# Kernel tuning notes

Hardware: AMD Instinct MI355X
Metric: run time of the kernel (lower is better)

## Reference

```python
import jax, jax.numpy as jnp
import numpy as np

B, LQ, LK = 8, 512, 512
DQ = DK = DV = 512
H = 128


def setup_inputs() -> dict:
    key = jax.random.key(0)
    kq, kk, kv, k1, k2, k3 = jax.random.split(key, 6)
    query = jax.random.normal(kq, (B, LQ, DQ), dtype=jnp.float32)
    key_t = jax.random.normal(kk, (B, LK, DK), dtype=jnp.float32)
    value = jax.random.normal(kv, (B, LK, DV), dtype=jnp.float32)
    # Linear weights stored torch-style as (out_features, in_features)
    w1 = jax.random.normal(k1, (H, DQ), dtype=jnp.float32) / np.sqrt(DQ)
    w2 = jax.random.normal(k2, (H, DK), dtype=jnp.float32) / np.sqrt(DK)
    v = jax.random.normal(k3, (1, H), dtype=jnp.float32) / np.sqrt(H)
    return {"query": query, "key": key_t, "value": value, "w1": w1, "w2": w2, "v": v}


def reference(query, key, value, w1, w2, v):
    # Linear projections first (mathematically identical to projecting the
    # broadcast tensors, since Linear is linear): (B,Lq,H), (B,Lk,H)
    q_proj = jnp.einsum("bqd,hd->bqh", query, w1)
    k_proj = jnp.einsum("bkd,hd->bkh", key, w2)
    # Broadcast add -> tanh -> project to scalar: (B,Lq,Lk,H) intermediate
    feat = jnp.tanh(q_proj[:, :, None, :] + k_proj[:, None, :, :])
    score = jnp.einsum("bqkh,h->bqk", feat, v[0])
    attention_weights = jax.nn.softmax(score, axis=-1)
    context_vector = jnp.einsum("bqk,bkv->bqv", attention_weights, value)
    return (attention_weights, context_vector)
```

## Files before the change

kernel.cpp:

```cpp
#include <hip/hip_runtime.h>

#define TWO_LOG2E 2.8853900817779268f

__device__ __forceinline__ float frcp(float x) {
#if __has_builtin(__builtin_amdgcn_rcpf)
  return __builtin_amdgcn_rcpf(x);
#else
  return 1.0f / x;
#endif
}
__device__ __forceinline__ float fexp2(float x) {
#if __has_builtin(__builtin_amdgcn_exp2f)
  return __builtin_amdgcn_exp2f(x);
#else
  return exp2f(x);
#endif
}
__device__ __forceinline__ unsigned short f2bf(float f) {
  unsigned int u = __float_as_uint(f);
  u += 0x7fffu + ((u >> 16) & 1u);
  return (unsigned short)(u >> 16);
}
__device__ __forceinline__ unsigned int pack2bf(float lo, float hi) {
  return (unsigned int)f2bf(lo) | ((unsigned int)f2bf(hi) << 16);
}

using short8 = __attribute__((ext_vector_type(8))) short;
using f32x4v = __attribute__((ext_vector_type(4))) float;
using f32x8s = __attribute__((ext_vector_type(8))) float;
using f32x2 = __attribute__((ext_vector_type(2))) float;

__device__ __forceinline__ f32x2 pkfma(f32x2 a, f32x2 b, f32x2 c) {
  return __builtin_elementwise_fma(a, b, c);
}
__device__ __forceinline__ f32x2 splat2(float x) {
  f32x2 r;
  r.x = x;
  r.y = x;
  return r;
}
__device__ __forceinline__ f32x2 unpack_bf2(unsigned u) {
  f32x2 r;
  r.x = __uint_as_float(u << 16);
  r.y = __uint_as_float(u & 0xffff0000u);
  return r;
}
__device__ __forceinline__ void cell4k(float a0, float a1, float a2, float a3,
                                       f32x2 b0, f32x2 b1, f32x2 b2, f32x2 b3,
                                       float v0, float v1, float v2, float v3,
                                       f32x2& s) {
  const f32x2 one = {1.f, 1.f};
  f32x2 x0 = pkfma(splat2(a0), b0, one);
  f32x2 x1 = pkfma(splat2(a1), b1, one);
  f32x2 x2 = pkfma(splat2(a2), b2, one);
  f32x2 x3 = pkfma(splat2(a3), b3, one);
  f32x2 p01 = x0 * x1, p23 = x2 * x3;
  f32x2 n01 = pkfma(splat2(v0), x1, splat2(v1) * x0);
  f32x2 n23 = pkfma(splat2(v2), x3, splat2(v3) * x2);
  f32x2 num = pkfma(n01, p23, n23 * p01);
  f32x2 den = p01 * p23;
  f32x2 r;
  r.x = frcp(den.x);
  r.y = frcp(den.y);
  s = pkfma(num, r, s);
}

__global__ __launch_bounds__(256) void k_pre(
    const float* __restrict__ query, const float* __restrict__ key,
    const float* __restrict__ w1, const float* __restrict__ w2,
    const float* __restrict__ value,
    float* __restrict__ Aout, unsigned short* __restrict__ BoutT,
    unsigned short* __restrict__ valT) {
  __shared__ __align__(16) char Abuf[16 * 128];
  __shared__ __align__(16) char Bbuf[128 * 128];
  __shared__ unsigned short ts[64][66];

  const int t = threadIdx.x;

  if (blockIdx.y == 0) {
    const int px = blockIdx.x;
    const bool isB = px >= 256;
    const float* in = isB ? key : query;
    const float* wm = isB ? w2 : w1;
    const int m0g = (px & 255) * 16;
    const int w = t >> 6, l = t & 63;

    f32x4v acc[2];
    acc[0] = 0;
    acc[1] = 0;

    float4 aS;
    float4 wS[4][2];

#define P_LOAD(k0_)                                                        \
  {                                                                        \
    aS = *(const float4*)&in[(m0g + (t >> 4)) * 512 + (k0_) + (t & 15) * 4]; \
    _Pragma("unroll") for (int i = 0; i < 4; ++i) {                        \
      int tt = t + i * 256;                                                \
      int row = tt >> 3, g = tt & 7;                                       \
      const float* src = &wm[row * 512 + (k0_) + g * 8];                   \
      wS[i][0] = *(const float4*)src;                                      \
      wS[i][1] = *(const float4*)(src + 4);                                \
    }                                                                      \
  }
#define P_WRITE()                                                          \
  {                                                                        \
    int arow = t >> 4, q4 = t & 15;                                        \
    *(uint2*)(Abuf + arow * 128 + (((q4 >> 1) ^ (arow & 7)) << 4) +        \
              ((q4 & 1) << 3)) =                                           \
        make_uint2(pack2bf(aS.x, aS.y), pack2bf(aS.z, aS.w));              \
    _Pragma("unroll") for (int i = 0; i < 4; ++i) {                        \
      int tt = t + i * 256;                                                \
      int row = tt >> 3, g = tt & 7;                                       \
      uint4 p = make_uint4(                                                \
          pack2bf(wS[i][0].x, wS[i][0].y), pack2bf(wS[i][0].z, wS[i][0].w),\
          pack2bf(wS[i][1].x, wS[i][1].y), pack2bf(wS[i][1].z, wS[i][1].w));\
      *(uint4*)(Bbuf + row * 128 + ((g ^ (row & 7)) << 4)) = p;            \
    }                                                                      \
  }

    P_LOAD(0);
#pragma unroll
    for (int ks8 = 0; ks8 < 8; ++ks8) {
      if (ks8) __syncthreads();
      P_WRITE();
      if (ks8 < 7) P_LOAD(ks8 * 64 + 64);
      __syncthreads();
#pragma unroll
      for (int ks = 0; ks < 2; ++ks) {
        const int gb = ks * 4 + (l >> 4);
        const int ra = l & 15;
        short8 af = *(const short8*)(Abuf + ra * 128 + ((gb ^ (ra & 7)) << 4));
#pragma unroll
        for (int ni = 0; ni < 2; ++ni) {
          const int rb = w * 32 + ni * 16 + (l & 15);
          short8 bf_ = *(const short8*)(Bbuf + rb * 128 + ((gb ^ (rb & 7)) << 4));
          if (isB)
            acc[ni] = __builtin_amdgcn_mfma_f32_16x16x32_bf16(bf_, af, acc[ni], 0, 0, 0);
          else
            acc[ni] = __builtin_amdgcn_mfma_f32_16x16x32_bf16(af, bf_, acc[ni], 0, 0, 0);
        }
      }
    }
#undef P_LOAD
#undef P_WRITE
    if (!isB) {
#pragma unroll
      for (int ni = 0; ni < 2; ++ni) {
        int col = w * 32 + ni * 16 + (l & 15);
#pragma unroll
        for (int j = 0; j < 4; ++j) {
          int row = m0g + (l >> 4) * 4 + j;
          Aout[row * 128 + col] = fexp2(acc[ni][j] * TWO_LOG2E);
        }
      }
    } else {
      int m = m0g + (l & 15);
#pragma unroll
      for (int ni = 0; ni < 2; ++ni)
#pragma unroll
        for (int j = 0; j < 4; ++j) {
          int h = w * 32 + ni * 16 + (l >> 4) * 4 + j;
          BoutT[h * 4096 + m] = f2bf(fexp2(acc[ni][j] * TWO_LOG2E));
        }
    }
  } else {
    const int x = blockIdx.x;
    const int b = x >> 6, k0 = ((x >> 3) & 7) * 64, n0 = (x & 7) * 64;
    {
      int kr = t >> 4, n4 = (t & 15) * 4;
#pragma unroll
      for (int i = 0; i < 4; ++i) {
        float4 f =
            *(const float4*)&value[((b * 512) + k0 + kr + 16 * i) * 512 + n0 + n4];
        *(ushort4*)&ts[kr + 16 * i][n4] =
            make_ushort4(f2bf(f.x), f2bf(f.y), f2bf(f.z), f2bf(f.w));
      }
    }
    __syncthreads();
    {
      int nw = t >> 4, k4 = (t & 15) * 4;
#pragma unroll
      for (int i = 0; i < 4; ++i) {
        int n = nw + 16 * i;
        ushort4 o = make_ushort4(ts[k4 + 0][n], ts[k4 + 1][n], ts[k4 + 2][n],
                                 ts[k4 + 3][n]);
        *(ushort4*)&valT[((b * 512) + n0 + n) * 512 + k0 + k4] = o;
      }
    }
  }
}

__global__ __launch_bounds__(512, 8) void k_score_softmax(
    const float* __restrict__ Aexp, const unsigned short* __restrict__ BexpT,
    const float* __restrict__ vw, float* __restrict__ attn,
    unsigned short* __restrict__ attnBf) {
  __shared__ __align__(16) f32x2 part[512][4];
  __shared__ float red[8][4];

  const int tid = threadIdx.x;
  const int b = blockIdx.y;
  const int qbase = blockIdx.x * 4;
  const int wav = tid >> 6;
  const int hgrp = wav >> 2;
  const int kq = wav & 3;
  const int lane = tid & 63;

  const unsigned* const bbase32 = (const unsigned*)(BexpT + b * 512);
  const int kidx = kq * 64 + lane;

  const float* const pa0 =
      Aexp + __builtin_amdgcn_readfirstlane((b * 512 + qbase) * 128);
  const float* const pa1 = pa0 + 128;
  const float* const pa2 = pa0 + 256;
  const float* const pa3 = pa0 + 384;
  const float* const pv = vw;
  const unsigned hoff = (unsigned)__builtin_amdgcn_readfirstlane(hgrp * 256);

  f32x2 acc0 = {0.f, 0.f}, acc1 = {0.f, 0.f};
  f32x2 acc2 = {0.f, 0.f}, acc3 = {0.f, 0.f};

#pragma unroll
  for (int ch = 0; ch < 8; ++ch) {
    f32x8s sa0, sa1, sa2, sa3, sv;
    unsigned soff = hoff + (unsigned)(ch * 32);
    asm volatile(
        "s_load_dwordx8 %0, %5, %10\n\t"
        "s_load_dwordx8 %1, %6, %10\n\t"
        "s_load_dwordx8 %2, %7, %10\n\t"
        "s_load_dwordx8 %3, %8, %10\n\t"
        "s_load_dwordx8 %4, %9, %10"
        : "=&s"(sa0), "=&s"(sa1), "=&s"(sa2), "=&s"(sa3), "=&s"(sv)
        : "s"(pa0), "s"(pa1), "s"(pa2), "s"(pa3), "s"(pv), "s"(soff));

    unsigned u[8];
#pragma unroll
    for (int j = 0; j < 8; ++j)
      u[j] = bbase32[hgrp * 131072 + ch * 16384 + j * 2048 + kidx];

    asm volatile("s_waitcnt lgkmcnt(0)"
                 : "+s"(sa0), "+s"(sa1), "+s"(sa2), "+s"(sa3), "+s"(sv));

#pragma unroll
    for (int g = 0; g < 2; ++g) {
      f32x2 b0 = unpack_bf2(u[g * 4 + 0]);
      f32x2 b1 = unpack_bf2(u[g * 4 + 1]);
      f32x2 b2 = unpack_bf2(u[g * 4 + 2]);
      f32x2 b3 = unpack_bf2(u[g * 4 + 3]);
      const int h = g * 4;
      cell4k(sa0[h], sa0[h + 1], sa0[h + 2], sa0[h + 3], b0, b1, b2, b3,
             sv[h], sv[h + 1], sv[h + 2], sv[h + 3], acc0);
      cell4k(sa1[h], sa1[h + 1], sa1[h + 2], sa1[h + 3], b0, b1, b2, b3,
             sv[h], sv[h + 1], sv[h + 2], sv[h + 3], acc1);
      cell4k(sa2[h], sa2[h + 1], sa2[h + 2], sa2[h + 3], b0, b1, b2, b3,
             sv[h], sv[h + 1], sv[h + 2], sv[h + 3], acc2);
      cell4k(sa3[h], sa3[h + 1], sa3[h + 2], sa3[h + 3], b0, b1, b2, b3,
             sv[h], sv[h + 1], sv[h + 2], sv[h + 3], acc3);
    }
  }

  part[tid][0] = acc0;
  part[tid][1] = acc1;
  part[tid][2] = acc2;
  part[tid][3] = acc3;
  __syncthreads();
  {
    const f32x2* pp = part[tid ^ 256];
    acc0 += pp[0];
    acc1 += pp[1];
    acc2 += pp[2];
    acc3 += pp[3];
  }

  float P0e = fexp2(acc0.x * -TWO_LOG2E);
  float P0o = fexp2(acc0.y * -TWO_LOG2E);
  float P1e = fexp2(acc1.x * -TWO_LOG2E);
  float P1o = fexp2(acc1.y * -TWO_LOG2E);
  float P2e = fexp2(acc2.x * -TWO_LOG2E);
  float P2o = fexp2(acc2.y * -TWO_LOG2E);
  float P3e = fexp2(acc3.x * -TWO_LOG2E);
  float P3o = fexp2(acc3.y * -TWO_LOG2E);
  float s0 = P0e + P0o, s1 = P1e + P1o, s2 = P2e + P2o, s3 = P3e + P3o;
#pragma unroll
  for (int off = 32; off > 0; off >>= 1) {
    s0 += __shfl_xor(s0, off);
    s1 += __shfl_xor(s1, off);
    s2 += __shfl_xor(s2, off);
    s3 += __shfl_xor(s3, off);
  }
  if (lane == 0) {
    red[wav][0] = s0; red[wav][1] = s1; red[wav][2] = s2; red[wav][3] = s3;
  }
  __syncthreads();
  const int rb = hgrp * 4;
  float r0 = frcp(red[rb][0] + red[rb + 1][0] + red[rb + 2][0] + red[rb + 3][0]);
  float r1 = frcp(red[rb][1] + red[rb + 1][1] + red[rb + 2][1] + red[rb + 3][1]);
  float r2 = frcp(red[rb][2] + red[rb + 1][2] + red[rb + 2][2] + red[rb + 3][2]);
  float r3 = frcp(red[rb][3] + red[rb + 1][3] + red[rb + 2][3] + red[rb + 3][3]);

  const int row0 = (b * 512 + qbase) * 512;
  const int k0 = kidx * 2;
  if (hgrp == 0) {
    float a0e = P0e * r0, a0o = P0o * r0, a1e = P1e * r1, a1o = P1o * r1;
    *(float2*)&attn[row0 + k0] = make_float2(a0e, a0o);
    *(float2*)&attn[row0 + 512 + k0] = make_float2(a1e, a1o);
    *(unsigned*)&attnBf[row0 + k0] = pack2bf(a0e, a0o);
    *(unsigned*)&attnBf[row0 + 512 + k0] = pack2bf(a1e, a1o);
  } else {
    float a2e = P2e * r2, a2o = P2o * r2, a3e = P3e * r3, a3o = P3o * r3;
    *(float2*)&attn[row0 + 1024 + k0] = make_float2(a2e, a2o);
    *(float2*)&attn[row0 + 1536 + k0] = make_float2(a3e, a3o);
    *(unsigned*)&attnBf[row0 + 1024 + k0] = pack2bf(a2e, a2o);
    *(unsigned*)&attnBf[row0 + 1536 + k0] = pack2bf(a3e, a3o);
  }
}

__global__ __launch_bounds__(256) void k_context_mfma(
    const unsigned short* __restrict__ attnBf,
    const unsigned short* __restrict__ valT, float* __restrict__ ctx) {
  __shared__ __align__(16) char At[64 * 128];
  __shared__ __align__(16) char Bt[32 * 128];

  const int t = threadIdx.x;
  const int b = blockIdx.z;
  const int m0 = blockIdx.y * 64, n0 = blockIdx.x * 32;
  const int w = t >> 6, l = t & 63;
  const int wr = w >> 1, wc = w & 1;

  f32x4v acc[2];
  acc[0] = 0;
  acc[1] = 0;

  const int sr = t >> 2;
  const int sg = (t & 3);
  const int sswz = sr & 7;
  const int rbs = t >> 3;
  const int gbs = t & 7;

  for (int k0 = 0; k0 < 512; k0 += 64) {
    if (k0) __syncthreads();
    {
      const unsigned short* srca = &attnBf[(b * 512 + m0 + sr) * 512 + k0];
      char* dst = At + sr * 128;
#pragma unroll
      for (int h = 0; h < 2; ++h) {
        int g = sg * 2 + h;
        uint4 va = *(const uint4*)(srca + g * 8);
        *(uint4*)(dst + ((g ^ sswz) << 4)) = va;
      }
      uint4 vb = *(const uint4*)&valT[(b * 512 + n0 + rbs) * 512 + k0 + gbs * 8];
      *(uint4*)(Bt + rbs * 128 + ((gbs ^ (rbs & 7)) << 4)) = vb;
    }
    __syncthreads();
#pragma unroll
    for (int ks = 0; ks < 2; ++ks) {
      const int gb = ks * 4 + (l >> 4);
      const int rb = wc * 16 + (l & 15);
      short8 bf_ = *(const short8*)(Bt + rb * 128 + ((gb ^ (rb & 7)) << 4));
#pragma unroll
      for (int mi = 0; mi < 2; ++mi) {
        int ra = wr * 32 + mi * 16 + (l & 15);
        short8 af = *(const short8*)(At + ra * 128 + ((gb ^ (ra & 7)) << 4));
        acc[mi] = __builtin_amdgcn_mfma_f32_16x16x32_bf16(af, bf_, acc[mi], 0, 0, 0);
      }
    }
  }
  __syncthreads();
#pragma unroll
  for (int mi = 0; mi < 2; ++mi) {
    int col = n0 + wc * 16 + (l & 15);
#pragma unroll
    for (int j = 0; j < 4; ++j) {
      int row = m0 + wr * 32 + mi * 16 + (l >> 4) * 4 + j;
      ctx[(b * 512 + row) * 512 + col] = acc[mi][j];
    }
  }
}

extern "C" void kernel_launch(void* const* d_in, const int* in_sizes, int n_in,
                              void* d_out, int out_size, void* d_ws, size_t ws_size,
                              hipStream_t stream) {
  const float* query = (const float*)d_in[0];
  const float* key   = (const float*)d_in[1];
  const float* value = (const float*)d_in[2];
  const float* w1    = (const float*)d_in[3];
  const float* w2    = (const float*)d_in[4];
  const float* v     = (const float*)d_in[5];

  float* attn = (float*)d_out;
  float* ctx  = attn + 8 * 512 * 512;

  float* Aexp = (float*)d_ws;
  unsigned short* BexpT = (unsigned short*)(Aexp + 4096 * 128);
  unsigned short* valT = BexpT + 128 * 4096;
  unsigned short* attnBf = valT + 8 * 512 * 512;

  k_pre<<<dim3(512, 2), 256, 0, stream>>>(query, key, w1, w2, value,
                                          Aexp, BexpT, valT);
  k_score_softmax<<<dim3(128, 8), 512, 0, stream>>>(Aexp, BexpT, v, attn, attnBf);
  k_context_mfma<<<dim3(16, 8, 8), 256, 0, stream>>>(attnBf, valT, ctx);
}
```

Before: 52.21 us.

## Process eight query rows per block in score-softmax kernel to reuse key loads

The score/softmax kernel now computes eight query rows per block instead of four. Each block loads the bf16 key-projection data once and reuses it across twice as many rows, which halves that traffic per row. The scalar loads use immediate offsets from a per-head-group base pointer. The grid is halved and launch bounds are lowered to 4 blocks per SIMD/CU. More accumulators and SGPRs are live per thread, so occupancy and latency hiding may drop.

```diff
diff --git a/kernel.cpp b/kernel.cpp
--- a/kernel.cpp
+++ b/kernel.cpp
@@ -191,16 +191,16 @@
   }
 }
 
-__global__ __launch_bounds__(512, 8) void k_score_softmax(
+__global__ __launch_bounds__(512, 4) void k_score_softmax(
     const float* __restrict__ Aexp, const unsigned short* __restrict__ BexpT,
     const float* __restrict__ vw, float* __restrict__ attn,
     unsigned short* __restrict__ attnBf) {
-  __shared__ __align__(16) f32x2 part[512][4];
-  __shared__ float red[8][4];
+  __shared__ __align__(16) f32x2 part[512][8];
+  __shared__ float red[8][8];
 
   const int tid = threadIdx.x;
   const int b = blockIdx.y;
-  const int qbase = blockIdx.x * 4;
+  const int qbase = blockIdx.x * 8;
   const int wav = tid >> 6;
   const int hgrp = wav >> 2;
   const int kq = wav & 3;
@@ -208,110 +208,143 @@
 
   const unsigned* const bbase32 = (const unsigned*)(BexpT + b * 512);
   const int kidx = kq * 64 + lane;
-
-  const float* const pa0 =
-      Aexp + __builtin_amdgcn_readfirstlane((b * 512 + qbase) * 128);
-  const float* const pa1 = pa0 + 128;
-  const float* const pa2 = pa0 + 256;
-  const float* const pa3 = pa0 + 384;
-  const float* const pv = vw;
-  const unsigned hoff = (unsigned)__builtin_amdgcn_readfirstlane(hgrp * 256);
-
-  f32x2 acc0 = {0.f, 0.f}, acc1 = {0.f, 0.f};
-  f32x2 acc2 = {0.f, 0.f}, acc3 = {0.f, 0.f};
-
-#pragma unroll
-  for (int ch = 0; ch < 8; ++ch) {
-    f32x8s sa0, sa1, sa2, sa3, sv;
-    unsigned soff = hoff + (unsigned)(ch * 32);
-    asm volatile(
-        "s_load_dwordx8 %0, %5, %10\n\t"
-        "s_load_dwordx8 %1, %6, %10\n\t"
-        "s_load_dwordx8 %2, %7, %10\n\t"
-        "s_load_dwordx8 %3, %8, %10\n\t"
-        "s_load_dwordx8 %4, %9, %10"
-        : "=&s"(sa0), "=&s"(sa1), "=&s"(sa2), "=&s"(sa3), "=&s"(sv)
-        : "s"(pa0), "s"(pa1), "s"(pa2), "s"(pa3), "s"(pv), "s"(soff));
-
-    unsigned u[8];
-#pragma unroll
-    for (int j = 0; j < 8; ++j)
-      u[j] = bbase32[hgrp * 131072 + ch * 16384 + j * 2048 + kidx];
-
-    asm volatile("s_waitcnt lgkmcnt(0)"
-                 : "+s"(sa0), "+s"(sa1), "+s"(sa2), "+s"(sa3), "+s"(sv));
-
-#pragma unroll
-    for (int g = 0; g < 2; ++g) {
-      f32x2 b0 = unpack_bf2(u[g * 4 + 0]);
-      f32x2 b1 = unpack_bf2(u[g * 4 + 1]);
-      f32x2 b2 = unpack_bf2(u[g * 4 + 2]);
-      f32x2 b3 = unpack_bf2(u[g * 4 + 3]);
-      const int h = g * 4;
-      cell4k(sa0[h], sa0[h + 1], sa0[h + 2], sa0[h + 3], b0, b1, b2, b3,
-             sv[h], sv[h + 1], sv[h + 2], sv[h + 3], acc0);
-      cell4k(sa1[h], sa1[h + 1], sa1[h + 2], sa1[h + 3], b0, b1, b2, b3,
-             sv[h], sv[h + 1], sv[h + 2], sv[h + 3], acc1);
-      cell4k(sa2[h], sa2[h + 1], sa2[h + 2], sa2[h + 3], b0, b1, b2, b3,
-             sv[h], sv[h + 1], sv[h + 2], sv[h + 3], acc2);
-      cell4k(sa3[h], sa3[h + 1], sa3[h + 2], sa3[h + 3], b0, b1, b2, b3,
-             sv[h], sv[h + 1], sv[h + 2], sv[h + 3], acc3);
-    }
-  }
-
-  part[tid][0] = acc0;
-  part[tid][1] = acc1;
-  part[tid][2] = acc2;
-  part[tid][3] = acc3;
+  const int hbase = hgrp * 131072;
+
+  const float* const pah =
+      Aexp + __builtin_amdgcn_readfirstlane((b * 512 + qbase) * 128 + hgrp * 64);
+  const float* const pvh = vw + __builtin_amdgcn_readfirstlane(hgrp * 64);
+
+  f32x2 c0 = {0.f, 0.f}, c1 = {0.f, 0.f}, c2 = {0.f, 0.f}, c3 = {0.f, 0.f};
+  f32x2 c4 = {0.f, 0.f}, c5 = {0.f, 0.f}, c6 = {0.f, 0.f}, c7 = {0.f, 0.f};
+
+#define K2_CHUNK(CH_)                                                      \
+  {                                                                        \
+    f32x8s sa0, sa1, sa2, sa3, sa4, sa5, sa6, sa7, sv;                     \
+    asm volatile(                                                          \
+        "s_load_dwordx8 %0, %9, %11\n\t"                                   \
+        "s_load_dwordx8 %1, %9, %12\n\t"                                   \
+        "s_load_dwordx8 %2, %9, %13\n\t"                                   \
+        "s_load_dwordx8 %3, %9, %14\n\t"                                   \
+        "s_load_dwordx8 %4, %9, %15\n\t"                                   \
+        "s_load_dwordx8 %5, %9, %16\n\t"                                   \
+        "s_load_dwordx8 %6, %9, %17\n\t"                                   \
+        "s_load_dwordx8 %7, %9, %18\n\t"                                   \
+        "s_load_dwordx8 %8, %10, %11"                                      \
+        : "=&s"(sa0), "=&s"(sa1), "=&s"(sa2), "=&s"(sa3), "=&s"(sa4),      \
+          "=&s"(sa5), "=&s"(sa6), "=&s"(sa7), "=&s"(sv)                    \
+        : "s"(pah), "s"(pvh), "i"((CH_)*32), "i"((CH_)*32 + 512),          \
+          "i"((CH_)*32 + 1024), "i"((CH_)*32 + 1536), "i"((CH_)*32 + 2048),\
+          "i"((CH_)*32 + 2560), "i"((CH_)*32 + 3072),                      \
+          "i"((CH_)*32 + 3584));                                           \
+    unsigned u[8];                                                         \
+    _Pragma("unroll") for (int j = 0; j < 8; ++j)                          \
+        u[j] = bbase32[hbase + (CH_)*16384 + j * 2048 + kidx];             \
+    asm volatile("s_waitcnt lgkmcnt(0)"                                    \
+                 : "+s"(sa0), "+s"(sa1), "+s"(sa2), "+s"(sa3), "+s"(sa4),  \
+                   "+s"(sa5), "+s"(sa6), "+s"(sa7), "+s"(sv));             \
+    _Pragma("unroll") for (int g = 0; g < 2; ++g) {                        \
+      f32x2 b0 = unpack_bf2(u[g * 4 + 0]);                                 \
+      f32x2 b1 = unpack_bf2(u[g * 4 + 1]);                                 \
+      f32x2 b2 = unpack_bf2(u[g * 4 + 2]);                                 \
+      f32x2 b3 = unpack_bf2(u[g * 4 + 3]);                                 \
+      const int h = g * 4;                                                 \
+      cell4k(sa0[h], sa0[h + 1], sa0[h + 2], sa0[h + 3], b0, b1, b2, b3,   \
+             sv[h], sv[h + 1], sv[h + 2], sv[h + 3], c0);                  \
+      cell4k(sa1[h], sa1[h + 1], sa1[h + 2], sa1[h + 3], b0, b1, b2, b3,   \
+             sv[h], sv[h + 1], sv[h + 2], sv[h + 3], c1);                  \
+      cell4k(sa2[h], sa2[h + 1], sa2[h + 2], sa2[h + 3], b0, b1, b2, b3,   \
+             sv[h], sv[h + 1], sv[h + 2], sv[h + 3], c2);                  \
+      cell4k(sa3[h], sa3[h + 1], sa3[h + 2], sa3[h + 3], b0, b1, b2, b3,   \
+             sv[h], sv[h + 1], sv[h + 2], sv[h + 3], c3);                  \
+      cell4k(sa4[h], sa4[h + 1], sa4[h + 2], sa4[h + 3], b0, b1, b2, b3,   \
+             sv[h], sv[h + 1], sv[h + 2], sv[h + 3], c4);                  \
+      cell4k(sa5[h], sa5[h + 1], sa5[h + 2], sa5[h + 3], b0, b1, b2, b3,   \
+             sv[h], sv[h + 1], sv[h + 2], sv[h + 3], c5);                  \
+      cell4k(sa6[h], sa6[h + 1], sa6[h + 2], sa6[h + 3], b0, b1, b2, b3,   \
+             sv[h], sv[h + 1], sv[h + 2], sv[h + 3], c6);                  \
+      cell4k(sa7[h], sa7[h + 1], sa7[h + 2], sa7[h + 3], b0, b1, b2, b3,   \
+             sv[h], sv[h + 1], sv[h + 2], sv[h + 3], c7);                  \
+    }                                                                      \
+  }
+
+  K2_CHUNK(0)
+  K2_CHUNK(1)
+  K2_CHUNK(2)
+  K2_CHUNK(3)
+  K2_CHUNK(4)
+  K2_CHUNK(5)
+  K2_CHUNK(6)
+  K2_CHUNK(7)
+#undef K2_CHUNK
+
+  part[tid][0] = c0; part[tid][1] = c1; part[tid][2] = c2; part[tid][3] = c3;
+  part[tid][4] = c4; part[tid][5] = c5; part[tid][6] = c6; part[tid][7] = c7;
   __syncthreads();
   {
     const f32x2* pp = part[tid ^ 256];
-    acc0 += pp[0];
-    acc1 += pp[1];
-    acc2 += pp[2];
-    acc3 += pp[3];
-  }
-
-  float P0e = fexp2(acc0.x * -TWO_LOG2E);
-  float P0o = fexp2(acc0.y * -TWO_LOG2E);
-  float P1e = fexp2(acc1.x * -TWO_LOG2E);
-  float P1o = fexp2(acc1.y * -TWO_LOG2E);
-  float P2e = fexp2(acc2.x * -TWO_LOG2E);
-  float P2o = fexp2(acc2.y * -TWO_LOG2E);
-  float P3e = fexp2(acc3.x * -TWO_LOG2E);
-  float P3o = fexp2(acc3.y * -TWO_LOG2E);
+    c0 += pp[0]; c1 += pp[1]; c2 += pp[2]; c3 += pp[3];
+    c4 += pp[4]; c5 += pp[5]; c6 += pp[6]; c7 += pp[7];
+  }
+
+  float P0e = fexp2(c0.x * -TWO_LOG2E), P0o = fexp2(c0.y * -TWO_LOG2E);
+  float P1e = fexp2(c1.x * -TWO_LOG2E), P1o = fexp2(c1.y * -TWO_LOG2E);
+  float P2e = fexp2(c2.x * -TWO_LOG2E), P2o = fexp2(c2.y * -TWO_LOG2E);
+  float P3e = fexp2(c3.x * -TWO_LOG2E), P3o = fexp2(c3.y * -TWO_LOG2E);
+  float P4e = fexp2(c4.x * -TWO_LOG2E), P4o = fexp2(c4.y * -TWO_LOG2E);
+  float P5e = fexp2(c5.x * -TWO_LOG2E), P5o = fexp2(c5.y * -TWO_LOG2E);
+  float P6e = fexp2(c6.x * -TWO_LOG2E), P6o = fexp2(c6.y * -TWO_LOG2E);
+  float P7e = fexp2(c7.x * -TWO_LOG2E), P7o = fexp2(c7.y * -TWO_LOG2E);
   float s0 = P0e + P0o, s1 = P1e + P1o, s2 = P2e + P2o, s3 = P3e + P3o;
+  float s4 = P4e + P4o, s5 = P5e + P5o, s6 = P6e + P6o, s7 = P7e + P7o;
 #pragma unroll
   for (int off = 32; off > 0; off >>= 1) {
     s0 += __shfl_xor(s0, off);
     s1 += __shfl_xor(s1, off);
     s2 += __shfl_xor(s2, off);
     s3 += __shfl_xor(s3, off);
+    s4 += __shfl_xor(s4, off);
+    s5 += __shfl_xor(s5, off);
+    s6 += __shfl_xor(s6, off);
+    s7 += __shfl_xor(s7, off);
   }
   if (lane == 0) {
     red[wav][0] = s0; red[wav][1] = s1; red[wav][2] = s2; red[wav][3] = s3;
+    red[wav][4] = s4; red[wav][5] = s5; red[wav][6] = s6; red[wav][7] = s7;
   }
   __syncthreads();
   const int rb = hgrp * 4;
-  float r0 = frcp(red[rb][0] + red[rb + 1][0] + red[rb + 2][0] + red[rb + 3][0]);
-  float r1 = frcp(red[rb][1] + red[rb + 1][1] + red[rb + 2][1] + red[rb + 3][1]);
-  float r2 = frcp(red[rb][2] + red[rb + 1][2] + red[rb + 2][2] + red[rb + 3][2]);
-  float r3 = frcp(red[rb][3] + red[rb + 1][3] + red[rb + 2][3] + red[rb + 3][3]);
-
   const int row0 = (b * 512 + qbase) * 512;
   const int k0 = kidx * 2;
   if (hgrp == 0) {
+    float r0 = frcp(red[rb][0] + red[rb + 1][0] + red[rb + 2][0] + red[rb + 3][0]);
+    float r1 = frcp(red[rb][1] + red[rb + 1][1] + red[rb + 2][1] + red[rb + 3][1]);
+    float r2 = frcp(red[rb][2] + red[rb + 1][2] + red[rb + 2][2] + red[rb + 3][2]);
+    float r3 = frcp(red[rb][3] + red[rb + 1][3] + red[rb + 2][3] + red[rb + 3][3]);
     float a0e = P0e * r0, a0o = P0o * r0, a1e = P1e * r1, a1o = P1o * r1;
+    float a2e = P2e * r2, a2o = P2o * r2, a3e = P3e * r3, a3o = P3o * r3;
     *(float2*)&attn[row0 + k0] = make_float2(a0e, a0o);
     *(float2*)&attn[row0 + 512 + k0] = make_float2(a1e, a1o);
+    *(float2*)&attn[row0 + 1024 + k0] = make_float2(a2e, a2o);
+    *(float2*)&attn[row0 + 1536 + k0] = make_float2(a3e, a3o);
     *(unsigned*)&attnBf[row0 + k0] = pack2bf(a0e, a0o);
     *(unsigned*)&attnBf[row0 + 512 + k0] = pack2bf(a1e, a1o);
-  } else {
-    float a2e = P2e * r2, a2o = P2o * r2, a3e = P3e * r3, a3o = P3o * r3;
-    *(float2*)&attn[row0 + 1024 + k0] = make_float2(a2e, a2o);
-    *(float2*)&attn[row0 + 1536 + k0] = make_float2(a3e, a3o);
     *(unsigned*)&attnBf[row0 + 1024 + k0] = pack2bf(a2e, a2o);
     *(unsigned*)&attnBf[row0 + 1536 + k0] = pack2bf(a3e, a3o);
+  } else {
+    float r4 = frcp(red[rb][4] + red[rb + 1][4] + red[rb + 2][4] + red[rb + 3][4]);
+    float r5 = frcp(red[rb][5] + red[rb + 1][5] + red[rb + 2][5] + red[rb + 3][5]);
+    float r6 = frcp(red[rb][6] + red[rb + 1][6] + red[rb + 2][6] + red[rb + 3][6]);
+    float r7 = frcp(red[rb][7] + red[rb + 1][7] + red[rb + 2][7] + red[rb + 3][7]);
+    float a4e = P4e * r4, a4o = P4o * r4, a5e = P5e * r5, a5o = P5o * r5;
+    float a6e = P6e * r6, a6o = P6o * r6, a7e = P7e * r7, a7o = P7o * r7;
+    *(float2*)&attn[row0 + 2048 + k0] = make_float2(a4e, a4o);
+    *(float2*)&attn[row0 + 2560 + k0] = make_float2(a5e, a5o);
+    *(float2*)&attn[row0 + 3072 + k0] = make_float2(a6e, a6o);
+    *(float2*)&attn[row0 + 3584 + k0] = make_float2(a7e, a7o);
+    *(unsigned*)&attnBf[row0 + 2048 + k0] = pack2bf(a4e, a4o);
+    *(unsigned*)&attnBf[row0 + 2560 + k0] = pack2bf(a5e, a5o);
+    *(unsigned*)&attnBf[row0 + 3072 + k0] = pack2bf(a6e, a6o);
+    *(unsigned*)&attnBf[row0 + 3584 + k0] = pack2bf(a7e, a7o);
   }
 }
 
@@ -397,6 +430,6 @@
 
   k_pre<<<dim3(512, 2), 256, 0, stream>>>(query, key, w1, w2, value,
                                           Aexp, BexpT, valT);
-  k_score_softmax<<<dim3(128, 8), 512, 0, stream>>>(Aexp, BexpT, v, attn, attnBf);
+  k_score_softmax<<<dim3(64, 8), 512, 0, stream>>>(Aexp, BexpT, v, attn, attnBf);
   k_context_mfma<<<dim3(16, 8, 8), 256, 0, stream>>>(attnBf, valT, ctx);
 }
```

Result: no change. 51.86 us (-0.7%).
